# Performance work log

Measured on AMD Instinct MI355X. Metric: run time of the kernel, lower is better.

Reference implementation:

```python
import jax, jax.numpy as jnp
import numpy as np

HEADS = 2
HID = 128
IN_DIM = 128
OUT_DIM = 1
N_NODES = 50000
NEG_SLOPE = 0.2  # PyG GATConv default
EPS = 1e-16


def setup_inputs() -> dict:
    key = jax.random.key(0)
    ks = jax.random.split(key, 16)
    N, E = N_NODES, 800000
    x = jax.random.normal(ks[0], (N, IN_DIM), dtype=jnp.float32)
    edge_index = jax.random.randint(ks[1], (2, E), 0, N, dtype=jnp.int32)
    s = 0.1
    # GATConv 1: in=128 -> heads=2, out=128 per head
    W1 = jax.random.normal(ks[2], (IN_DIM, HEADS * HID), dtype=jnp.float32) * s
    a_src1 = jax.random.normal(ks[3], (HEADS, HID), dtype=jnp.float32) * s
    a_dst1 = jax.random.normal(ks[4], (HEADS, HID), dtype=jnp.float32) * s
    b1 = jnp.zeros((HEADS * HID,), dtype=jnp.float32)
    # GATConv 2: in=256 -> heads=2, out=128 per head
    W2 = jax.random.normal(ks[5], (HEADS * HID, HEADS * HID), dtype=jnp.float32) * s
    a_src2 = jax.random.normal(ks[6], (HEADS, HID), dtype=jnp.float32) * s
    a_dst2 = jax.random.normal(ks[7], (HEADS, HID), dtype=jnp.float32) * s
    b2 = jnp.zeros((HEADS * HID,), dtype=jnp.float32)
    # post_mp: Linear(256,128) -> Dropout -> Linear(128,1)
    Wp1 = jax.random.normal(ks[8], (HEADS * HID, HID), dtype=jnp.float32) * s
    bp1 = jnp.zeros((HID,), dtype=jnp.float32)
    Wp2 = jax.random.normal(ks[9], (HID, OUT_DIM), dtype=jnp.float32) * s
    bp2 = jnp.zeros((OUT_DIM,), dtype=jnp.float32)
    return {"x": x, "edge_index": edge_index,
            "W1": W1, "a_src1": a_src1, "a_dst1": a_dst1, "b1": b1,
            "W2": W2, "a_src2": a_src2, "a_dst2": a_dst2, "b2": b2,
            "Wp1": Wp1, "bp1": bp1, "Wp2": Wp2, "bp2": bp2}


def gat_conv(x, src, dst, W, a_src, a_dst, b, num_nodes):
    """PyG-style GATConv (concat=True). src/dst already include self-loops."""
    N = num_nodes
    h = (x @ W).reshape(N, HEADS, HID)                        # [N,H,C]
    alpha_s = jnp.einsum('nhc,hc->nh', h, a_src)              # [N,H]
    alpha_d = jnp.einsum('nhc,hc->nh', h, a_dst)              # [N,H]
    e = jax.nn.leaky_relu(alpha_s[src] + alpha_d[dst], NEG_SLOPE)  # [E,H]
    # segment softmax over destination node
    emax = jax.ops.segment_max(e, dst, num_segments=N)        # [N,H]
    emax = jnp.where(jnp.isfinite(emax), emax, 0.0)
    w = jnp.exp(e - emax[dst])                                # [E,H]
    denom = jax.ops.segment_sum(w, dst, num_segments=N)       # [N,H]
    alpha = w / (denom[dst] + EPS)                            # [E,H]
    out = jax.ops.segment_sum(h[src] * alpha[:, :, None], dst, num_segments=N)
    return out.reshape(N, HEADS * HID) + b


def reference(x, edge_index, W1, a_src1, a_dst1, b1, W2, a_src2, a_dst2, b2,
              Wp1, bp1, Wp2, bp2):
    N = x.shape[0]
    loops = jnp.arange(N, dtype=edge_index.dtype)
    src = jnp.concatenate([edge_index[0], loops])
    dst = jnp.concatenate([edge_index[1], loops])
    h = gat_conv(x, src, dst, W1, a_src1, a_dst1, b1, N)
    h = jax.nn.relu(h)  # dropout is identity in eval mode
    h = gat_conv(h, src, dst, W2, a_src2, a_dst2, b2, N)
    h = jax.nn.relu(h)
    h = h @ Wp1 + bp1
    h = h @ Wp2 + bp2
    return jax.nn.sigmoid(h)
```

## Files before the change

kernel.cpp:

```cpp
#include <hip/hip_runtime.h>

#define HID 128
#define C2 256
#define NEG 0.2f
#define L2E 1.44269504088896340736f

typedef __bf16 v8bf __attribute__((ext_vector_type(8)));
typedef float  v4f  __attribute__((ext_vector_type(4)));
typedef float  v2f  __attribute__((ext_vector_type(2)));
typedef unsigned short us8 __attribute__((ext_vector_type(8)));

__device__ __forceinline__ float bf2f(unsigned short u) {
    union { float f; unsigned int i; } v; v.i = ((unsigned int)u) << 16; return v.f;
}
__device__ __forceinline__ unsigned short f2bf(float f) {
    union { float f; unsigned int i; } v; v.f = f;
    unsigned int r = v.i + 0x7FFFu + ((v.i >> 16) & 1u);
    return (unsigned short)(r >> 16);
}
__device__ __forceinline__ float lrelu(float x) { return x > 0.f ? x : NEG * x; }

__device__ __forceinline__ void packB_body(const float* __restrict__ W,
                                           unsigned short* __restrict__ out,
                                           int K, int N, int idx) {
    int ksteps = K >> 5;
    int total = (N >> 4) * ksteps * 64;
    if (idx >= total) return;
    int lane = idx & 63;
    int rest = idx >> 6;
    int tt = rest / ksteps, k0 = rest - tt * ksteps;
    int n = (tt >> 3) * 128 + (lane & 15) * 8 + (tt & 7);
    int kb = k0 * 32 + (lane >> 4) * 8;
    us8 v;
#pragma unroll
    for (int j = 0; j < 8; ++j) v[j] = f2bf(W[(size_t)(kb + j) * N + n]);
    *(us8*)(out + (size_t)idx * 8) = v;
}

__global__ __launch_bounds__(256) void prep_kernel(const float* __restrict__ W1, unsigned short* W1p,
                                                   const float* __restrict__ W2, unsigned short* W2p,
                                                   const float* __restrict__ Wp1, unsigned short* Wp1p,
                                                   const int* __restrict__ ei, int* __restrict__ cnt,
                                                   int* __restrict__ rank, int E,
                                                   int b1, int b2, int b3) {
    int b = blockIdx.x;
    if (b < b1) { packB_body(W1, W1p, HID, C2, b * 256 + threadIdx.x); return; }
    b -= b1;
    if (b < b2) { packB_body(W2, W2p, C2, C2, b * 256 + threadIdx.x); return; }
    b -= b2;
    if (b < b3) { packB_body(Wp1, Wp1p, C2, HID, b * 256 + threadIdx.x); return; }
    b -= b3;
    int i = b * 256 + threadIdx.x;
    if (i >= E) return;
    int d = ei[E + i];
    rank[i] = atomicAdd(&cnt[d], 1);
}

__global__ __launch_bounds__(256) void scanA(const int* __restrict__ cnt, int* __restrict__ rs,
                                             int* __restrict__ part, int N) {
    __shared__ int s[256];
    int t = threadIdx.x, i = blockIdx.x * 256 + t;
    int v = (i < N) ? cnt[i] : 0;
    s[t] = v; __syncthreads();
    for (int off = 1; off < 256; off <<= 1) {
        int x = (t >= off) ? s[t - off] : 0;
        __syncthreads();
        s[t] += x;
        __syncthreads();
    }
    if (i < N) rs[i] = s[t] - v;
    if (t == 255) part[blockIdx.x] = s[255];
}

__global__ __launch_bounds__(256) void scanB(int* __restrict__ part, int n) {
    __shared__ int s[256];
    int t = threadIdx.x;
    int v = (t < n) ? part[t] : 0;
    s[t] = v; __syncthreads();
    for (int off = 1; off < 256; off <<= 1) {
        int x = (t >= off) ? s[t - off] : 0;
        __syncthreads();
        s[t] += x;
        __syncthreads();
    }
    if (t < n) part[t] = s[t] - v;
}

__global__ void scanC(int* __restrict__ rs, const int* __restrict__ part, int N, int E) {
    int i = blockIdx.x * 256 + threadIdx.x;
    if (i < N) rs[i] += part[blockIdx.x];
    if (i == 0) rs[N] = E;
}

template<bool AFP32, int G>
__global__ __launch_bounds__(256) void gemm_alpha(const void* __restrict__ Av,
                                                  const unsigned short* __restrict__ Bp,
                                                  const float* __restrict__ asrc,
                                                  const float* __restrict__ adst,
                                                  float* __restrict__ asd,
                                                  unsigned char* __restrict__ C,
                                                  int M, int N, int K, int gemmBlocks,
                                                  const int* __restrict__ ei,
                                                  const int* __restrict__ rs,
                                                  const int* __restrict__ rank,
                                                  int* __restrict__ csr, int E) {
    if (blockIdx.x >= gemmBlocks) {
        int i = (blockIdx.x - gemmBlocks) * 256 + threadIdx.x;
        if (i < E) {
            int s = ei[i], d = ei[E + i];
            csr[rs[d] + rank[i]] = s;
        }
        return;
    }
    int ksteps = K >> 5;
    int ngrp = N >> 7;
    int mtiles = M >> 4;
    int w = (blockIdx.x << 2) + (threadIdx.x >> 6);
    int groups = (mtiles + G - 1) / G;
    int mp = w / ngrp, g = w - mp * ngrp;
    if (mp >= groups) return;
    int lane = threadIdx.x & 63;
    int l16 = lane & 15, quad = lane >> 4;
    int mt0 = mp * G;

    int mrow[G];
#pragma unroll
    for (int gi = 0; gi < G; ++gi) {
        int mt = mt0 + gi;
        mrow[gi] = (mt < mtiles ? mt : mtiles - 1) * 16 + l16;
    }

    const unsigned short* Bf = Bp + ((size_t)(g * 8) * ksteps << 9) + lane * 8;
    v4f acc[G][8];
#pragma unroll
    for (int gi = 0; gi < G; ++gi)
#pragma unroll
        for (int t = 0; t < 8; ++t) acc[gi][t] = (v4f){0, 0, 0, 0};

    for (int k0 = 0; k0 < ksteps; ++k0) {
        v8bf a[G];
        if (AFP32) {
            const float* A = (const float*)Av;
#pragma unroll
            for (int gi = 0; gi < G; ++gi) {
                const float* p = A + (size_t)mrow[gi] * K + k0 * 32 + quad * 8;
                float4 u0 = *(const float4*)p, u1 = *(const float4*)(p + 4);
                a[gi][0]=(__bf16)u0.x; a[gi][1]=(__bf16)u0.y; a[gi][2]=(__bf16)u0.z; a[gi][3]=(__bf16)u0.w;
                a[gi][4]=(__bf16)u1.x; a[gi][5]=(__bf16)u1.y; a[gi][6]=(__bf16)u1.z; a[gi][7]=(__bf16)u1.w;
            }
        } else {
            const unsigned short* A = (const unsigned short*)Av;
#pragma unroll
            for (int gi = 0; gi < G; ++gi)
                a[gi] = *(const v8bf*)(A + (size_t)mrow[gi] * K + k0 * 32 + quad * 8);
        }
#pragma unroll
        for (int t = 0; t < 8; ++t) {
            v8bf bfr = *(const v8bf*)(Bf + ((size_t)(t * ksteps + k0) << 9));
#pragma unroll
            for (int gi = 0; gi < G; ++gi)
                acc[gi][t] = __builtin_amdgcn_mfma_f32_16x16x32_bf16(a[gi], bfr, acc[gi][t], 0, 0, 0);
        }
    }

    int n0 = g << 7;
    int cb = n0 + l16 * 8;
    float sv[8], dv[8];
#pragma unroll
    for (int t = 0; t < 8; ++t) {
        sv[t] = asrc[cb + t];
        dv[t] = adst[cb + t];
    }
#pragma unroll
    for (int gi = 0; gi < G; ++gi) {
        int mt = mt0 + gi;
        if (mt >= mtiles) break;
        int row0 = mt * 16 + quad * 4;
#pragma unroll
        for (int r = 0; r < 4; ++r) {
            float sa = 0.f, sd = 0.f;
#pragma unroll
            for (int t = 0; t < 8; ++t) {
                sa += acc[gi][t][r] * sv[t];
                sd += acc[gi][t][r] * dv[t];
            }
            unsigned int w0 = __builtin_amdgcn_cvt_pk_fp8_f32(acc[gi][0][r], acc[gi][1][r], 0, false);
            w0 = __builtin_amdgcn_cvt_pk_fp8_f32(acc[gi][2][r], acc[gi][3][r], w0, true);
            unsigned int w1 = __builtin_amdgcn_cvt_pk_fp8_f32(acc[gi][4][r], acc[gi][5][r], 0, false);
            w1 = __builtin_amdgcn_cvt_pk_fp8_f32(acc[gi][6][r], acc[gi][7][r], w1, true);
            *(uint2*)(C + (size_t)(row0 + r) * N + cb) = (uint2){w0, w1};
#pragma unroll
            for (int off = 8; off; off >>= 1) {
                sa += __shfl_xor(sa, off);
                sd += __shfl_xor(sd, off);
            }
            if (l16 == 0) {
                int row = row0 + r;
                asd[(size_t)row * 4 + g]     = sa * L2E;
                asd[(size_t)row * 4 + 2 + g] = sd * L2E;
            }
        }
    }
}

__global__ __launch_bounds__(256) void agg_kernel(const int* __restrict__ rs,
                                                  const int* __restrict__ csr,
                                                  const unsigned char* __restrict__ h,
                                                  const float* __restrict__ asd,
                                                  const float* __restrict__ bias,
                                                  unsigned short* __restrict__ out, int N) {
    int d = blockIdx.x * 4 + (threadIdx.x >> 6);
    if (d >= N) return;
    int lane = threadIdx.x & 63;
    int beg = rs[d], end = rs[d + 1];
    int e4 = lane >> 4;
    int sub = lane & 15;
    int head = sub >> 3;
    float adh = asd[(size_t)d * 4 + 2 + head];
    int cbase = sub * 16;
    const unsigned char* hc = h + cbase;
    v2f acc[8];
#pragma unroll
    for (int j = 0; j < 8; ++j) acc[j] = (v2f){0, 0};
    float den = 0.f;
#pragma unroll 2
    for (int i = beg; i < end; i += 4) {
        int ei = i + e4;
        bool valid = ei < end;
        int s = csr[valid ? ei : end - 1];
        float e = lrelu(asd[(size_t)s * 4 + head] + adh);
        float wgt = valid ? __builtin_amdgcn_exp2f(e) : 0.f;
        den += wgt;
        uint4 u = *(const uint4*)(hc + (size_t)s * C2);
        v2f w2 = {wgt, wgt};
        acc[0] += w2 * __builtin_amdgcn_cvt_pk_f32_fp8(u.x, false);
        acc[1] += w2 * __builtin_amdgcn_cvt_pk_f32_fp8(u.x, true);
        acc[2] += w2 * __builtin_amdgcn_cvt_pk_f32_fp8(u.y, false);
        acc[3] += w2 * __builtin_amdgcn_cvt_pk_f32_fp8(u.y, true);
        acc[4] += w2 * __builtin_amdgcn_cvt_pk_f32_fp8(u.z, false);
        acc[5] += w2 * __builtin_amdgcn_cvt_pk_f32_fp8(u.z, true);
        acc[6] += w2 * __builtin_amdgcn_cvt_pk_f32_fp8(u.w, false);
        acc[7] += w2 * __builtin_amdgcn_cvt_pk_f32_fp8(u.w, true);
    }
    float a[16];
#pragma unroll
    for (int j = 0; j < 8; ++j) { a[2 * j] = acc[j].x; a[2 * j + 1] = acc[j].y; }
#pragma unroll
    for (int j = 0; j < 16; ++j) a[j] += __shfl_xor(a[j], 16);
#pragma unroll
    for (int j = 0; j < 16; ++j) a[j] += __shfl_xor(a[j], 32);
    den += __shfl_xor(den, 16);
    den += __shfl_xor(den, 32);
    if (e4 == 0) {
        float wS = __builtin_amdgcn_exp2f(lrelu(asd[(size_t)d * 4 + head] + adh));
        uint4 u = *(const uint4*)(hc + (size_t)d * C2);
        v2f p;
        p = __builtin_amdgcn_cvt_pk_f32_fp8(u.x, false); a[0]  += wS * p.x; a[1]  += wS * p.y;
        p = __builtin_amdgcn_cvt_pk_f32_fp8(u.x, true);  a[2]  += wS * p.x; a[3]  += wS * p.y;
        p = __builtin_amdgcn_cvt_pk_f32_fp8(u.y, false); a[4]  += wS * p.x; a[5]  += wS * p.y;
        p = __builtin_amdgcn_cvt_pk_f32_fp8(u.y, true);  a[6]  += wS * p.x; a[7]  += wS * p.y;
        p = __builtin_amdgcn_cvt_pk_f32_fp8(u.z, false); a[8]  += wS * p.x; a[9]  += wS * p.y;
        p = __builtin_amdgcn_cvt_pk_f32_fp8(u.z, true);  a[10] += wS * p.x; a[11] += wS * p.y;
        p = __builtin_amdgcn_cvt_pk_f32_fp8(u.w, false); a[12] += wS * p.x; a[13] += wS * p.y;
        p = __builtin_amdgcn_cvt_pk_f32_fp8(u.w, true);  a[14] += wS * p.x; a[15] += wS * p.y;
        float rden = 1.f / (den + wS + 1e-16f);
        us8 o0, o1;
#pragma unroll
        for (int j = 0; j < 8; ++j) o0[j] = f2bf(fmaxf(a[j] * rden + bias[cbase + j], 0.f));
#pragma unroll
        for (int j = 0; j < 8; ++j) o1[j] = f2bf(fmaxf(a[8 + j] * rden + bias[cbase + 8 + j], 0.f));
        *(us8*)(out + (size_t)d * C2 + cbase) = o0;
        *(us8*)(out + (size_t)d * C2 + cbase + 8) = o1;
    }
}

template<int G>
__global__ __launch_bounds__(256) void gemm_final(const unsigned short* __restrict__ A,
                                                  const unsigned short* __restrict__ Bp,
                                                  const float* __restrict__ bp1,
                                                  const float* __restrict__ wp2,
                                                  const float* __restrict__ bp2,
                                                  float* __restrict__ out,
                                                  int M, int K) {
    int ksteps = K >> 5;
    int mtiles = M >> 4;
    int groups = (mtiles + G - 1) / G;
    int mp = (blockIdx.x << 2) + (threadIdx.x >> 6);
    if (mp >= groups) return;
    int lane = threadIdx.x & 63;
    int l16 = lane & 15, quad = lane >> 4;

    int mrow[G];
#pragma unroll
    for (int gi = 0; gi < G; ++gi) {
        int mt = mp * G + gi;
        mrow[gi] = (mt < mtiles ? mt : mtiles - 1) * 16 + l16;
    }

    const unsigned short* Bf = Bp + lane * 8;
    v4f acc[G][8];
#pragma unroll
    for (int gi = 0; gi < G; ++gi)
#pragma unroll
        for (int t = 0; t < 8; ++t) acc[gi][t] = (v4f){0, 0, 0, 0};
    for (int k0 = 0; k0 < ksteps; ++k0) {
        v8bf a[G];
#pragma unroll
        for (int gi = 0; gi < G; ++gi)
            a[gi] = *(const v8bf*)(A + (size_t)mrow[gi] * K + k0 * 32 + quad * 8);
#pragma unroll
        for (int t = 0; t < 8; ++t) {
            v8bf bfr = *(const v8bf*)(Bf + ((size_t)(t * ksteps + k0) << 9));
#pragma unroll
            for (int gi = 0; gi < G; ++gi)
                acc[gi][t] = __builtin_amdgcn_mfma_f32_16x16x32_bf16(a[gi], bfr, acc[gi][t], 0, 0, 0);
        }
    }
    int cb = l16 * 8;
    float wv8[8], bv[8];
#pragma unroll
    for (int t = 0; t < 8; ++t) {
        wv8[t] = wp2[cb + t];
        bv[t] = bp1[cb + t];
    }
    float bias2 = bp2[0];
#pragma unroll
    for (int gi = 0; gi < G; ++gi) {
        int mt = mp * G + gi;
        if (mt >= mtiles) break;
        int row0 = mt * 16 + quad * 4;
#pragma unroll
        for (int r = 0; r < 4; ++r) {
            float s = 0.f;
#pragma unroll
            for (int t = 0; t < 8; ++t) s += (acc[gi][t][r] + bv[t]) * wv8[t];
#pragma unroll
            for (int off = 8; off; off >>= 1) s += __shfl_xor(s, off);
            if (l16 == 0) {
                float xv = s + bias2;
                out[row0 + r] = 1.f / (1.f + __expf(-xv));
            }
        }
    }
}

extern "C" void kernel_launch(void* const* d_in, const int* in_sizes, int n_in,
                              void* d_out, int out_size, void* d_ws, size_t ws_size,
                              hipStream_t stream) {
    const float* x   = (const float*)d_in[0];
    const int*   ei  = (const int*)d_in[1];
    const float* W1  = (const float*)d_in[2];
    const float* as1 = (const float*)d_in[3];
    const float* ad1 = (const float*)d_in[4];
    const float* b1  = (const float*)d_in[5];
    const float* W2  = (const float*)d_in[6];
    const float* as2 = (const float*)d_in[7];
    const float* ad2 = (const float*)d_in[8];
    const float* b2  = (const float*)d_in[9];
    const float* Wp1 = (const float*)d_in[10];
    const float* bp1 = (const float*)d_in[11];
    const float* Wp2 = (const float*)d_in[12];
    const float* bp2 = (const float*)d_in[13];
    float* out = (float*)d_out;

    int NN = in_sizes[0] / HID;
    int E  = in_sizes[1] / 2;

    char* ws = (char*)d_ws;
    size_t off = 0;
    auto alloc = [&](size_t bytes) -> char* {
        char* p = ws + off;
        off += (bytes + 255) & ~(size_t)255;
        return p;
    };
    unsigned char*  bufH = (unsigned char*)alloc((size_t)NN * C2);
    unsigned short* bufO = (unsigned short*)alloc((size_t)NN * C2 * 2);
    float* asd = (float*)alloc((size_t)NN * 4 * sizeof(float));
    int* rs    = (int*)alloc((size_t)(NN + 1) * 4);
    int* cnt   = (int*)alloc((size_t)NN * 4);
    int* rank  = (int*)alloc((size_t)E * 4);
    int* csr   = (int*)alloc((size_t)E * 4);
    int* part  = (int*)alloc(1024);
    unsigned short* W1p  = (unsigned short*)alloc((size_t)HID * C2 * 2);
    unsigned short* W2p  = (unsigned short*)alloc((size_t)C2 * C2 * 2);
    unsigned short* Wp1p = (unsigned short*)alloc((size_t)C2 * HID * 2);

    int nchunk = (NN + 255) / 256;
    int eblk   = (E + 255) / 256;

    int pb1 = (HID * C2 / 8 + 255) / 256;
    int pb2 = (C2 * C2 / 8 + 255) / 256;
    int pb3 = (C2 * HID / 8 + 255) / 256;
    hipMemsetAsync(cnt, 0, (size_t)NN * 4, stream);
    prep_kernel<<<pb1 + pb2 + pb3 + eblk, 256, 0, stream>>>(W1, W1p, W2, W2p, Wp1, Wp1p,
                                                            ei, cnt, rank, E, pb1, pb2, pb3);
    scanA<<<nchunk, 256, 0, stream>>>(cnt, rs, part, NN);
    scanB<<<1, 256, 0, stream>>>(part, nchunk);
    scanC<<<nchunk, 256, 0, stream>>>(rs, part, NN, E);

    const int G = 2;
    int mtiles = NN / 16;
    int groups = (mtiles + G - 1) / G;
    int gemmBlocks = (groups * 2 + 3) / 4;
    int aggGrid = (NN + 3) / 4;

    gemm_alpha<true, G><<<gemmBlocks + eblk, 256, 0, stream>>>(x, W1p, as1, ad1, asd, bufH,
                                                               NN, C2, HID, gemmBlocks,
                                                               ei, rs, rank, csr, E);
    agg_kernel<<<aggGrid, 256, 0, stream>>>(rs, csr, bufH, asd, b1, bufO, NN);
    gemm_alpha<false, G><<<gemmBlocks, 256, 0, stream>>>(bufO, W2p, as2, ad2, asd, bufH,
                                                         NN, C2, C2, gemmBlocks,
                                                         nullptr, nullptr, nullptr, nullptr, 0);
    agg_kernel<<<aggGrid, 256, 0, stream>>>(rs, csr, bufH, asd, b2, bufO, NN);
    gemm_final<G><<<(groups + 3) / 4, 256, 0, stream>>>(bufO, Wp1p, bp1, Wp2, bp2, out, NN, C2);
}
```

Before: 283.2 us.

## Batch edge index and weight loads per warp in aggregation; unroll GEMM K loops

The aggregation kernel now loads 32 CSR neighbor indices and computes both heads' attention weights cooperatively across the wavefront, then broadcasts them with shuffles. Previously each lane group loaded indices and computed exp per step, which serialized dependent gathers. Separately, GEMM kernels get the K step count as a template parameter, fully unroll the K loop and preload all B fragments before issuing MFMAs, to improve latency hiding. The unrolling raises register pressure, and the shuffle approach adds a second level of loop overhead.

```diff
diff --git a/kernel.cpp b/kernel.cpp
--- a/kernel.cpp
+++ b/kernel.cpp
@@ -92,14 +92,14 @@
     if (i == 0) rs[N] = E;
 }
 
-template<bool AFP32, int G>
+template<bool AFP32, int G, int KSTEPS>
 __global__ __launch_bounds__(256) void gemm_alpha(const void* __restrict__ Av,
                                                   const unsigned short* __restrict__ Bp,
                                                   const float* __restrict__ asrc,
                                                   const float* __restrict__ adst,
                                                   float* __restrict__ asd,
                                                   unsigned char* __restrict__ C,
-                                                  int M, int N, int K, int gemmBlocks,
+                                                  int M, int N, int gemmBlocks,
                                                   const int* __restrict__ ei,
                                                   const int* __restrict__ rs,
                                                   const int* __restrict__ rank,
@@ -112,7 +112,7 @@
         }
         return;
     }
-    int ksteps = K >> 5;
+    constexpr int K = KSTEPS * 32;
     int ngrp = N >> 7;
     int mtiles = M >> 4;
     int w = (blockIdx.x << 2) + (threadIdx.x >> 6);
@@ -130,14 +130,19 @@
         mrow[gi] = (mt < mtiles ? mt : mtiles - 1) * 16 + l16;
     }
 
-    const unsigned short* Bf = Bp + ((size_t)(g * 8) * ksteps << 9) + lane * 8;
+    const unsigned short* Bf = Bp + ((size_t)(g * 8) * KSTEPS << 9) + lane * 8;
     v4f acc[G][8];
 #pragma unroll
     for (int gi = 0; gi < G; ++gi)
 #pragma unroll
         for (int t = 0; t < 8; ++t) acc[gi][t] = (v4f){0, 0, 0, 0};
 
-    for (int k0 = 0; k0 < ksteps; ++k0) {
+#pragma unroll
+    for (int k0 = 0; k0 < KSTEPS; ++k0) {
+        v8bf bfr[8];
+#pragma unroll
+        for (int t = 0; t < 8; ++t)
+            bfr[t] = *(const v8bf*)(Bf + ((size_t)(t * KSTEPS + k0) << 9));
         v8bf a[G];
         if (AFP32) {
             const float* A = (const float*)Av;
@@ -155,12 +160,10 @@
                 a[gi] = *(const v8bf*)(A + (size_t)mrow[gi] * K + k0 * 32 + quad * 8);
         }
 #pragma unroll
-        for (int t = 0; t < 8; ++t) {
-            v8bf bfr = *(const v8bf*)(Bf + ((size_t)(t * ksteps + k0) << 9));
+        for (int t = 0; t < 8; ++t)
 #pragma unroll
             for (int gi = 0; gi < G; ++gi)
-                acc[gi][t] = __builtin_amdgcn_mfma_f32_16x16x32_bf16(a[gi], bfr, acc[gi][t], 0, 0, 0);
-        }
+                acc[gi][t] = __builtin_amdgcn_mfma_f32_16x16x32_bf16(a[gi], bfr[t], acc[gi][t], 0, 0, 0);
     }
 
     int n0 = g << 7;
@@ -216,31 +219,43 @@
     int e4 = lane >> 4;
     int sub = lane & 15;
     int head = sub >> 3;
-    float adh = asd[(size_t)d * 4 + 2 + head];
+    int l32 = lane & 31;
+    int whead = lane >> 5;
+    float adh0 = asd[(size_t)d * 4 + 2];
+    float adh1 = asd[(size_t)d * 4 + 3];
+    float adh  = head  ? adh1 : adh0;
+    float wadh = whead ? adh1 : adh0;
     int cbase = sub * 16;
     const unsigned char* hc = h + cbase;
     v2f acc[8];
 #pragma unroll
     for (int j = 0; j < 8; ++j) acc[j] = (v2f){0, 0};
     float den = 0.f;
+    for (int c0 = beg; c0 < end; c0 += 32) {
+        int ce = c0 + l32;
+        bool av = ce < end;
+        int s_w = csr[av ? ce : end - 1];
+        float e_w = lrelu(asd[(size_t)s_w * 4 + whead] + wadh);
+        float w_w = av ? __builtin_amdgcn_exp2f(e_w) : 0.f;
+        int rem = end - c0; if (rem > 32) rem = 32;
+        int iters = (rem + 3) >> 2;
 #pragma unroll 2
-    for (int i = beg; i < end; i += 4) {
-        int ei = i + e4;
-        bool valid = ei < end;
-        int s = csr[valid ? ei : end - 1];
-        float e = lrelu(asd[(size_t)s * 4 + head] + adh);
-        float wgt = valid ? __builtin_amdgcn_exp2f(e) : 0.f;
-        den += wgt;
-        uint4 u = *(const uint4*)(hc + (size_t)s * C2);
-        v2f w2 = {wgt, wgt};
-        acc[0] += w2 * __builtin_amdgcn_cvt_pk_f32_fp8(u.x, false);
-        acc[1] += w2 * __builtin_amdgcn_cvt_pk_f32_fp8(u.x, true);
-        acc[2] += w2 * __builtin_amdgcn_cvt_pk_f32_fp8(u.y, false);
-        acc[3] += w2 * __builtin_amdgcn_cvt_pk_f32_fp8(u.y, true);
-        acc[4] += w2 * __builtin_amdgcn_cvt_pk_f32_fp8(u.z, false);
-        acc[5] += w2 * __builtin_amdgcn_cvt_pk_f32_fp8(u.z, true);
-        acc[6] += w2 * __builtin_amdgcn_cvt_pk_f32_fp8(u.w, false);
-        acc[7] += w2 * __builtin_amdgcn_cvt_pk_f32_fp8(u.w, true);
+        for (int it = 0; it < iters; ++it) {
+            int j = (it << 2) + e4;
+            int   s   = __shfl(s_w, j);
+            float wgt = __shfl(w_w, j + (head << 5));
+            den += wgt;
+            uint4 u = *(const uint4*)(hc + ((size_t)s << 8));
+            v2f w2 = {wgt, wgt};
+            acc[0] += w2 * __builtin_amdgcn_cvt_pk_f32_fp8(u.x, false);
+            acc[1] += w2 * __builtin_amdgcn_cvt_pk_f32_fp8(u.x, true);
+            acc[2] += w2 * __builtin_amdgcn_cvt_pk_f32_fp8(u.y, false);
+            acc[3] += w2 * __builtin_amdgcn_cvt_pk_f32_fp8(u.y, true);
+            acc[4] += w2 * __builtin_amdgcn_cvt_pk_f32_fp8(u.z, false);
+            acc[5] += w2 * __builtin_amdgcn_cvt_pk_f32_fp8(u.z, true);
+            acc[6] += w2 * __builtin_amdgcn_cvt_pk_f32_fp8(u.w, false);
+            acc[7] += w2 * __builtin_amdgcn_cvt_pk_f32_fp8(u.w, true);
+        }
     }
     float a[16];
 #pragma unroll
@@ -274,15 +289,15 @@
     }
 }
 
-template<int G>
+template<int G, int KSTEPS>
 __global__ __launch_bounds__(256) void gemm_final(const unsigned short* __restrict__ A,
                                                   const unsigned short* __restrict__ Bp,
                                                   const float* __restrict__ bp1,
                                                   const float* __restrict__ wp2,
                                                   const float* __restrict__ bp2,
                                                   float* __restrict__ out,
-                                                  int M, int K) {
-    int ksteps = K >> 5;
+                                                  int M) {
+    constexpr int K = KSTEPS * 32;
     int mtiles = M >> 4;
     int groups = (mtiles + G - 1) / G;
     int mp = (blockIdx.x << 2) + (threadIdx.x >> 6);
@@ -303,18 +318,21 @@
     for (int gi = 0; gi < G; ++gi)
 #pragma unroll
         for (int t = 0; t < 8; ++t) acc[gi][t] = (v4f){0, 0, 0, 0};
-    for (int k0 = 0; k0 < ksteps; ++k0) {
+#pragma unroll
+    for (int k0 = 0; k0 < KSTEPS; ++k0) {
+        v8bf bfr[8];
+#pragma unroll
+        for (int t = 0; t < 8; ++t)
+            bfr[t] = *(const v8bf*)(Bf + ((size_t)(t * KSTEPS + k0) << 9));
         v8bf a[G];
 #pragma unroll
         for (int gi = 0; gi < G; ++gi)
             a[gi] = *(const v8bf*)(A + (size_t)mrow[gi] * K + k0 * 32 + quad * 8);
 #pragma unroll
-        for (int t = 0; t < 8; ++t) {
-            v8bf bfr = *(const v8bf*)(Bf + ((size_t)(t * ksteps + k0) << 9));
+        for (int t = 0; t < 8; ++t)
 #pragma unroll
             for (int gi = 0; gi < G; ++gi)
-                acc[gi][t] = __builtin_amdgcn_mfma_f32_16x16x32_bf16(a[gi], bfr, acc[gi][t], 0, 0, 0);
-        }
+                acc[gi][t] = __builtin_amdgcn_mfma_f32_16x16x32_bf16(a[gi], bfr[t], acc[gi][t], 0, 0, 0);
     }
     int cb = l16 * 8;
     float wv8[8], bv[8];
@@ -404,13 +422,13 @@
     int gemmBlocks = (groups * 2 + 3) / 4;
     int aggGrid = (NN + 3) / 4;
 
-    gemm_alpha<true, G><<<gemmBlocks + eblk, 256, 0, stream>>>(x, W1p, as1, ad1, asd, bufH,
-                                                               NN, C2, HID, gemmBlocks,
-                                                               ei, rs, rank, csr, E);
+    gemm_alpha<true, G, 4><<<gemmBlocks + eblk, 256, 0, stream>>>(x, W1p, as1, ad1, asd, bufH,
+                                                                  NN, C2, gemmBlocks,
+                                                                  ei, rs, rank, csr, E);
     agg_kernel<<<aggGrid, 256, 0, stream>>>(rs, csr, bufH, asd, b1, bufO, NN);
-    gemm_alpha<false, G><<<gemmBlocks, 256, 0, stream>>>(bufO, W2p, as2, ad2, asd, bufH,
-                                                         NN, C2, C2, gemmBlocks,
-                                                         nullptr, nullptr, nullptr, nullptr, 0);
+    gemm_alpha<false, G, 8><<<gemmBlocks, 256, 0, stream>>>(bufO, W2p, as2, ad2, asd, bufH,
+                                                            NN, C2, gemmBlocks,
+                                                            nullptr, nullptr, nullptr, nullptr, 0);
     agg_kernel<<<aggGrid, 256, 0, stream>>>(rs, csr, bufH, asd, b2, bufO, NN);
-    gemm_final<G><<<(groups + 3) / 4, 256, 0, stream>>>(bufO, Wp1p, bp1, Wp2, bp2, out, NN, C2);
-}
+    gemm_final<G, 8><<<(groups + 3) / 4, 256, 0, stream>>>(bufO, Wp1p, bp1, Wp2, bp2, out, NN);
+}
```

After: 305.9 us. +8.0%, slower.
